# Kernel tuning notes

Measured on AMD Instinct MI355X. Metric: run time of the kernel, lower is better.

Reference implementation:

```python
import jax, jax.numpy as jnp
import numpy as np

N_VERT = 20000


def _gather_pad(feat, adj):
    # feat: [B, N, C]; adj: [B, N, K] with 1-based indices, 0 = padding (-> zeros)
    B, N, C = feat.shape
    padded = jnp.concatenate([jnp.zeros((B, 1, C), feat.dtype), feat], axis=1)  # [B, N+1, C]
    return jax.vmap(lambda p, a: p[a])(padded, adj)  # [B, N, K, C]


def setup_inputs() -> dict:
    key = jax.random.key(0)
    ks = jax.random.split(key, 7)
    B, N, K, M, C, O = 4, N_VERT, 16, 9, 64, 64
    x = jax.random.normal(ks[0], (B, N, C), jnp.float32)
    adj = jax.random.randint(ks[1], (B, N, K), 0, N + 1, jnp.int32)  # 0 == no neighbor
    W = jax.random.normal(ks[2], (M, O, C), jnp.float32) * 0.1
    b = jax.random.normal(ks[3], (O,), jnp.float32) * 0.1
    u = jax.random.normal(ks[4], (M, C), jnp.float32) * 0.1
    v = jax.random.normal(ks[5], (M, C), jnp.float32) * 0.1
    c = jax.random.normal(ks[6], (M,), jnp.float32) * 0.1
    return {"x": x, "adj": adj, "W": W, "b": b, "u": u, "v": v, "c": c}


def reference(x, adj, W, b, u, v, c):
    # FEAST graph conv, non-invariant path.
    mask = adj != 0  # [B, N, K]
    # attention logits: u.x_i + v.x_j + c, masked (padding) neighbors -> 0 + c
    ux = jnp.einsum('bnc,mc->bnm', x, u)          # [B, N, M]
    vx = jnp.einsum('bnc,mc->bnm', x, v)          # [B, N, M]
    vxn = _gather_pad(vx, adj)                    # [B, N, K, M]
    logits = jnp.where(mask[..., None], ux[:, :, None, :] + vxn, 0.0) + c
    q = jax.nn.softmax(logits, axis=-1)           # softmax over M kernels
    # gather raw neighbor features (zero for padding), contract q over K first,
    # then apply per-kernel W (linear, so order is equivalent to original wx-gather)
    xn = _gather_pad(x, adj)                      # [B, N, K, C]
    s = jnp.einsum('bnkm,bnkc->bnmc', q, xn)      # [B, N, M, C]
    out = jnp.einsum('bnmc,moc->bno', s, W)       # [B, N, O]
    deg = jnp.sum(mask, axis=-1).astype(x.dtype)  # [B, N]
    inv_deg = jnp.where(deg > 0, 1.0 / jnp.maximum(deg, 1.0), 0.0)
    return out * inv_deg[..., None] + b
```

## Files before the change

### kernel.cpp

```cpp
#include <hip/hip_runtime.h>
#include <cstdint>
#include <cstddef>

#define BB 4
#define NN 20000
#define KK 16
#define MM 9
#define CC 64
#define OO 64
#define BN (BB*NN)
#define MC (MM*CC)
#define NKS (MC/32)
#define NCH 625

typedef _Float16 f16x8 __attribute__((ext_vector_type(8)));
typedef _Float16 f16x4 __attribute__((ext_vector_type(4)));
typedef __fp16   fp16v2 __attribute__((ext_vector_type(2)));
typedef float    f32x4 __attribute__((ext_vector_type(4)));
typedef unsigned short u16;
typedef unsigned int   u32;

union Hcv { _Float16 h; u16 u; };
__device__ __forceinline__ u16 f2h(float f) { Hcv t; t.h = (_Float16)f; return t.u; }

__global__ __launch_bounds__(256) void pre_kernel(
    const float* __restrict__ x, const float* __restrict__ W,
    const float* __restrict__ u, const float* __restrict__ v,
    u16* __restrict__ xh, u16* __restrict__ wfb2, u16* __restrict__ uvfa)
{
    const int bid = blockIdx.x;
    if (bid == 1286) {
        int i0 = threadIdx.x * 8;
        u16 w8[8];
        #pragma unroll
        for (int tt = 0; tt < 8; ++tt) {
            int i = i0 + tt;
            int t = i >> 10, l = (i >> 4) & 63, s = (i >> 3) & 1, j = i & 7;
            int m = l & 15, hh = l >> 4;
            const float* src = t ? v : u;
            float val = (m < 9) ? src[m * 64 + s * 32 + hh * 8 + j] : 0.f;
            w8[tt] = f2h(val);
        }
        *(ushort4*)(uvfa + i0)     = *(ushort4*)(w8);
        *(ushort4*)(uvfa + i0 + 4) = *(ushort4*)(w8 + 4);
        return;
    }
    if (bid >= 1250) {
        int base = (bid - 1250) * 1024 + threadIdx.x * 4;
        ushort4 wv;
        u16* wp = (u16*)&wv;
        #pragma unroll
        for (int t = 0; t < 4; ++t) {
            int i = base + t;
            int j = i & 7, o = (i >> 3) & 63, l2 = (i >> 9) & 3, ks = i >> 11;
            int kf = ks * 32 + l2 * 8 + j;
            int m = kf >> 6, cc2 = kf & 63;
            wp[t] = f2h(W[m * 4096 + o * 64 + cc2]);
        }
        *(ushort4*)(wfb2 + base) = wv;
        return;
    }
    const int wave = threadIdx.x >> 6, lane = threadIdx.x & 63;
    const int lr = lane & 15, lhi = lane >> 4;
    const int t0n = bid * 64 + wave * 16;
    const float* xr = x + (size_t)(t0n + lr) * 64 + lhi * 8;
    float xf[16];
    *(float4*)(xf + 0)  = *(const float4*)(xr + 0);
    *(float4*)(xf + 4)  = *(const float4*)(xr + 4);
    *(float4*)(xf + 8)  = *(const float4*)(xr + 32);
    *(float4*)(xf + 12) = *(const float4*)(xr + 36);
    union { u16 us[8]; ushort4 s4[2]; } H0, H1;
    #pragma unroll
    for (int i = 0; i < 8; ++i) {
        H0.us[i] = f2h(xf[i]);
        H1.us[i] = f2h(xf[8 + i]);
    }
    u16* xw = xh + (size_t)(t0n + lr) * 64 + lhi * 8;
    *(ushort4*)(xw)          = H0.s4[0];
    *(ushort4*)(xw + 4)      = H0.s4[1];
    *(ushort4*)(xw + 32)     = H1.s4[0];
    *(ushort4*)(xw + 32 + 4) = H1.s4[1];
}

__global__ __launch_bounds__(256, 3) void fused_kernel(
    const u16* __restrict__ xh, const int* __restrict__ adj,
    const u16* __restrict__ wfb2, const u16* __restrict__ uvfa,
    const float* __restrict__ cvec, const float* __restrict__ bias,
    float* __restrict__ out)
{
    __shared__ __align__(16) u16 qlds[32 * 256];
    __shared__ __align__(16) u16 slds[72 * 32 * 8];
    const int bid = blockIdx.x;
    const int grp = bid & 7;
    const int b = grp >> 1;
    const int chunk = (bid >> 3) * 2 + (grp & 1);
    if (chunk >= NCH) return;
    const int tid = threadIdx.x, wave = tid >> 6, lane = tid & 63;
    const int lr = lane & 15, lhi = lane >> 4;
    const int node0 = b * NN + chunk * 32;
    const u16* xhb = xh + ((size_t)(b * NN) << 6);

    int jjA[2];
    jjA[0] = adj[(size_t)node0 * KK + tid];
    jjA[1] = adj[(size_t)node0 * KK + 256 + tid];

    f16x8 gLo[2][4], gHi[2][4];
    #pragma unroll
    for (int t = 0; t < 2; ++t)
        #pragma unroll
        for (int g2 = 0; g2 < 4; ++g2) {
            int e = __builtin_amdgcn_ds_bpermute((g2 * 16 + lr) * 4, jjA[t]);
            int erow = ((e > 0) ? e : 1) - 1;
            const u16* rp = xhb + ((size_t)erow << 6) + lhi * 8;
            gLo[t][g2] = *(const f16x8*)(rp);
            gHi[t][g2] = *(const f16x8*)(rp + 32);
        }

    const u16* up = uvfa + lane * 16;
    const f16x8 uAlo = *(const f16x8*)(up);
    const f16x8 uAhi = *(const f16x8*)(up + 8);
    const f16x8 vAlo = *(const f16x8*)(up + 1024);
    const f16x8 vAhi = *(const f16x8*)(up + 1024 + 8);
    float cv[4];
    #pragma unroll
    for (int r = 0; r < 4; ++r) { int m = lhi * 4 + r; cv[r] = (m < 9) ? cvec[m] : 0.f; }

    f16x8 idf[2];
    #pragma unroll
    for (int s = 0; s < 2; ++s) {
        union { u16 us[8]; f16x8 v; } t;
        #pragma unroll
        for (int j = 0; j < 8; ++j)
            t.us[j] = (lhi * 8 + j == s * 16 + lr) ? (u16)0x3C00 : (u16)0;
        idf[s] = t.v;
    }

    const int o0 = wave * 16;
    const float bv = bias[o0 + lr];
    const u32 qbase = (u32)(size_t)qlds;

    #pragma unroll
    for (int t = 0; t < 2; ++t) {
        unsigned long long bal = __ballot(jjA[t] != 0);
        #pragma unroll
        for (int g2 = 0; g2 < 4; ++g2) {
            const int nd = t * 16 + wave * 4 + g2;
            const u16* orp = xh + ((size_t)(node0 + nd) << 6) + lhi * 8;
            f16x8 oLo = *(const f16x8*)(orp);
            f16x8 oHi = *(const f16x8*)(orp + 32);
            f32x4 acc = {0.f, 0.f, 0.f, 0.f};
            acc = __builtin_amdgcn_mfma_f32_16x16x32_f16(vAlo, gLo[t][g2], acc, 0, 0, 0);
            acc = __builtin_amdgcn_mfma_f32_16x16x32_f16(vAhi, gHi[t][g2], acc, 0, 0, 0);
            acc = __builtin_amdgcn_mfma_f32_16x16x32_f16(uAlo, oLo, acc, 0, 0, 0);
            acc = __builtin_amdgcn_mfma_f32_16x16x32_f16(uAhi, oHi, acc, 0, 0, 0);
            u32 field = (u32)(bal >> (g2 * 16)) & 0xffffu;
            int  deg  = __popc(field);
            float inv = (deg > 0) ? __fdividef(1.0f, (float)deg) : 0.0f;
            int kbit = (field >> lr) & 1;
            float lm[4];
            #pragma unroll
            for (int r = 0; r < 4; ++r)
                lm[r] = (lhi * 4 + r < 9) ? (acc[r] + cv[r]) : -1e30f;
            float mx = fmaxf(fmaxf(lm[0], lm[1]), fmaxf(lm[2], lm[3]));
            mx = fmaxf(mx, __shfl_xor(mx, 16));
            mx = fmaxf(mx, __shfl_xor(mx, 32));
            float p0 = __expf(lm[0] - mx), p1 = __expf(lm[1] - mx);
            float p2 = __expf(lm[2] - mx), p3 = __expf(lm[3] - mx);
            float S = p0 + p1 + p2 + p3;
            S += __shfl_xor(S, 16);
            S += __shfl_xor(S, 32);
            float qsc = kbit ? __fdividef(inv, S) : 0.0f;
            union { fp16v2 h2[2]; uint2 u2; } qp;
            qp.h2[0] = __builtin_amdgcn_cvt_pkrtz(p0 * qsc, p1 * qsc);
            qp.h2[1] = __builtin_amdgcn_cvt_pkrtz(p2 * qsc, p3 * qsc);
            *(uint2*)(qlds + nd * 256 + lhi * 4 + (lr & 3) * 16 + (lr >> 2) * 64) = qp.u2;
        }
        asm volatile("s_waitcnt lgkmcnt(0)" ::: "memory");
        f16x4 qf[4];
        {
            u32 qa = qbase + (u32)((t * 16 + wave * 4) * 512) + (u32)(lane * 8);
            asm volatile("ds_read_b64_tr_b16 %0, %1 offset:0"    : "=v"(qf[0]) : "v"(qa) : "memory");
            asm volatile("ds_read_b64_tr_b16 %0, %1 offset:512"  : "=v"(qf[1]) : "v"(qa) : "memory");
            asm volatile("ds_read_b64_tr_b16 %0, %1 offset:1024" : "=v"(qf[2]) : "v"(qa) : "memory");
            asm volatile("ds_read_b64_tr_b16 %0, %1 offset:1536" : "=v"(qf[3]) : "v"(qa) : "memory");
            asm volatile("s_waitcnt lgkmcnt(0)" ::: "memory");
            __builtin_amdgcn_sched_barrier(0);
        }
        #pragma unroll
        for (int g2 = 0; g2 < 4; ++g2) {
            const int rnode = t * 16 + wave * 4 + g2;
            #pragma unroll
            for (int cc = 0; cc < 4; ++cc) {
                f32x4 xt = {0.f, 0.f, 0.f, 0.f};
                xt = __builtin_amdgcn_mfma_f32_16x16x32_f16(
                         (cc < 2) ? gLo[t][g2] : gHi[t][g2], idf[cc & 1], xt, 0, 0, 0);
                union { fp16v2 h2[2]; f16x4 h4; } at;
                at.h2[0] = __builtin_amdgcn_cvt_pkrtz(xt[0], xt[1]);
                at.h2[1] = __builtin_amdgcn_cvt_pkrtz(xt[2], xt[3]);
                f32x4 d2 = {0.f, 0.f, 0.f, 0.f};
                d2 = __builtin_amdgcn_mfma_f32_16x16x16f16(at.h4, qf[g2], d2, 0, 0, 0);
                if (lr < 9) {
                    u32 lo = __builtin_amdgcn_perm((u32)f2h(d2[1]), (u32)f2h(d2[0]), 0x05040100u);
                    u32 hi = __builtin_amdgcn_perm((u32)f2h(d2[3]), (u32)f2h(d2[2]), 0x05040100u);
                    int q_ = lr * 8 + cc * 2 + (lhi >> 1);
                    int idx = (((q_ * 32 + rnode) << 3) ^ ((lr & 7) << 3)) + (lhi & 1) * 4;
                    *(uint2*)(slds + idx) = make_uint2(lo, hi);
                }
            }
        }
    }
    __syncthreads();

    f32x4 a0 = {0.f, 0.f, 0.f, 0.f}, a1 = {0.f, 0.f, 0.f, 0.f};
    #pragma unroll
    for (int ks = 0; ks < NKS; ++ks) {
        int q_ = ks * 4 + lhi;
        int sw = ((q_ >> 3) & 7) << 3;
        f16x8 af0 = *(const f16x8*)(slds + ((((q_ * 32) + lr) << 3) ^ sw));
        f16x8 af1 = *(const f16x8*)(slds + ((((q_ * 32) + 16 + lr) << 3) ^ sw));
        f16x8 bf  = *(const f16x8*)(wfb2 + (size_t)(q_ * 64 + o0 + lr) * 8);
        a0 = __builtin_amdgcn_mfma_f32_16x16x32_f16(af0, bf, a0, 0, 0, 0);
        a1 = __builtin_amdgcn_mfma_f32_16x16x32_f16(af1, bf, a1, 0, 0, 0);
    }
    #pragma unroll
    for (int r = 0; r < 4; ++r) {
        out[(size_t)(node0 + lhi * 4 + r) * OO + o0 + lr]      = a0[r] + bv;
        out[(size_t)(node0 + 16 + lhi * 4 + r) * OO + o0 + lr] = a1[r] + bv;
    }
}

extern "C" void kernel_launch(void* const* d_in, const int* in_sizes, int n_in,
                              void* d_out, int out_size, void* d_ws, size_t ws_size,
                              hipStream_t stream)
{
    const float* x   = (const float*)d_in[0];
    const int*   adj = (const int*)  d_in[1];
    const float* W   = (const float*)d_in[2];
    const float* b   = (const float*)d_in[3];
    const float* u   = (const float*)d_in[4];
    const float* v   = (const float*)d_in[5];
    const float* c   = (const float*)d_in[6];
    float* out = (float*)d_out;

    u16* xh   = (u16*)d_ws;
    u16* wfb2 = xh + (size_t)BN * CC;
    u16* uvfa = wfb2 + 36864;

    pre_kernel<<<1287, 256, 0, stream>>>(x, W, u, v, xh, wfb2, uvfa);
    fused_kernel<<<2504, 256, 0, stream>>>(xh, adj, wfb2, uvfa, c, b, out);
}
```

Before: 134.8 us.

## Precompute u·x+c in pre-kernel and transpose gathered features via LDS reads

```diff
diff --git a/kernel.cpp b/kernel.cpp
--- a/kernel.cpp
+++ b/kernel.cpp
@@ -10,6 +10,7 @@
 #define OO 64
 #define BN (BB*NN)
 #define MC (MM*CC)
+#define UVP 12
 #define NKS (MC/32)
 #define NCH 625
 
@@ -22,27 +23,36 @@
 
 union Hcv { _Float16 h; u16 u; };
 __device__ __forceinline__ u16 f2h(float f) { Hcv t; t.h = (_Float16)f; return t.u; }
+__device__ __forceinline__ float h2f(u16 h) { Hcv t; t.u = h; return (float)t.h; }
+
+__device__ __forceinline__ f16x4 tr_read(u32 addr) {
+    f16x4 r;
+    asm volatile("ds_read_b64_tr_b16 %0, %1 offset:0" : "=v"(r) : "v"(addr) : "memory");
+    return r;
+}
 
 __global__ __launch_bounds__(256) void pre_kernel(
     const float* __restrict__ x, const float* __restrict__ W,
     const float* __restrict__ u, const float* __restrict__ v,
-    u16* __restrict__ xh, u16* __restrict__ wfb2, u16* __restrict__ uvfa)
+    const float* __restrict__ c,
+    float* __restrict__ uxcv, u16* __restrict__ xh,
+    u16* __restrict__ wfb2, u16* __restrict__ vfa)
 {
     const int bid = blockIdx.x;
     if (bid == 1286) {
-        int i0 = threadIdx.x * 8;
-        u16 w8[8];
-        #pragma unroll
-        for (int tt = 0; tt < 8; ++tt) {
-            int i = i0 + tt;
-            int t = i >> 10, l = (i >> 4) & 63, s = (i >> 3) & 1, j = i & 7;
-            int m = l & 15, hh = l >> 4;
-            const float* src = t ? v : u;
-            float val = (m < 9) ? src[m * 64 + s * 32 + hh * 8 + j] : 0.f;
-            w8[tt] = f2h(val);
-        }
-        *(ushort4*)(uvfa + i0)     = *(ushort4*)(w8);
-        *(ushort4*)(uvfa + i0 + 4) = *(ushort4*)(w8 + 4);
+        int i0 = threadIdx.x * 4;
+        if (i0 < 1024) {
+            u16 w4[4];
+            #pragma unroll
+            for (int tt = 0; tt < 4; ++tt) {
+                int i = i0 + tt;
+                int l = i >> 4, s = (i >> 3) & 1, j = i & 7;
+                int m = l & 15, hh = l >> 4;
+                float val = (m < 9) ? v[m * 64 + s * 32 + hh * 8 + j] : 0.f;
+                w4[tt] = f2h(val);
+            }
+            *(ushort4*)(vfa + i0) = *(ushort4*)(w4);
+        }
         return;
     }
     if (bid >= 1250) {
@@ -69,26 +79,55 @@
     *(float4*)(xf + 4)  = *(const float4*)(xr + 4);
     *(float4*)(xf + 8)  = *(const float4*)(xr + 32);
     *(float4*)(xf + 12) = *(const float4*)(xr + 36);
-    union { u16 us[8]; ushort4 s4[2]; } H0, H1;
+    union { u16 us[8]; f16x8 v; ushort4 s4[2]; } H0, L0, H1, L1;
     #pragma unroll
     for (int i = 0; i < 8; ++i) {
-        H0.us[i] = f2h(xf[i]);
-        H1.us[i] = f2h(xf[8 + i]);
+        u16 h = f2h(xf[i]);      H0.us[i] = h;  L0.us[i] = f2h(xf[i] - h2f(h));
+        u16 h2 = f2h(xf[8 + i]); H1.us[i] = h2; L1.us[i] = f2h(xf[8 + i] - h2f(h2));
     }
     u16* xw = xh + (size_t)(t0n + lr) * 64 + lhi * 8;
     *(ushort4*)(xw)          = H0.s4[0];
     *(ushort4*)(xw + 4)      = H0.s4[1];
     *(ushort4*)(xw + 32)     = H1.s4[0];
     *(ushort4*)(xw + 32 + 4) = H1.s4[1];
-}
-
-__global__ __launch_bounds__(256, 3) void fused_kernel(
+
+    f32x4 acc = {0.f,0.f,0.f,0.f};
+    const float* gp = u + lr * 64;
+    bool nz = lr < 9;
+    #pragma unroll
+    for (int s = 0; s < 2; ++s) {
+        float gf[8];
+        *(float4*)(gf + 0) = nz ? *(const float4*)(gp + s * 32 + lhi * 8)
+                                : make_float4(0.f,0.f,0.f,0.f);
+        *(float4*)(gf + 4) = nz ? *(const float4*)(gp + s * 32 + lhi * 8 + 4)
+                                : make_float4(0.f,0.f,0.f,0.f);
+        union { u16 us[8]; f16x8 v; } GH, GL;
+        #pragma unroll
+        for (int i = 0; i < 8; ++i) {
+            u16 h = f2h(gf[i]); GH.us[i] = h; GL.us[i] = f2h(gf[i] - h2f(h));
+        }
+        f16x8 as  = s ? H1.v : H0.v;
+        f16x8 asl = s ? L1.v : L0.v;
+        acc = __builtin_amdgcn_mfma_f32_16x16x32_f16(as,  GH.v, acc, 0, 0, 0);
+        acc = __builtin_amdgcn_mfma_f32_16x16x32_f16(as,  GL.v, acc, 0, 0, 0);
+        acc = __builtin_amdgcn_mfma_f32_16x16x32_f16(asl, GH.v, acc, 0, 0, 0);
+    }
+    float cv = (lr < 9) ? c[lr] : 0.f;
+    #pragma unroll
+    for (int reg = 0; reg < 4; ++reg) {
+        int node = t0n + lhi * 4 + reg;
+        if (lr < 9) uxcv[(size_t)node * UVP + lr] = acc[reg] + cv;
+    }
+}
+
+__global__ __launch_bounds__(256, 2) void fused_kernel(
     const u16* __restrict__ xh, const int* __restrict__ adj,
-    const u16* __restrict__ wfb2, const u16* __restrict__ uvfa,
-    const float* __restrict__ cvec, const float* __restrict__ bias,
+    const float* __restrict__ uxcv, const u16* __restrict__ wfb2,
+    const u16* __restrict__ vfa, const float* __restrict__ bias,
     float* __restrict__ out)
 {
-    __shared__ __align__(16) u16 qlds[32 * 256];
+    __shared__ __align__(16) u16 qlds[4 * 4 * 256];
+    __shared__ __align__(16) u16 xnlds[4 * 4 * 1024];
     __shared__ __align__(16) u16 slds[72 * 32 * 8];
     const int bid = blockIdx.x;
     const int grp = bid & 7;
@@ -116,43 +155,38 @@
             gHi[t][g2] = *(const f16x8*)(rp + 32);
         }
 
-    const u16* up = uvfa + lane * 16;
-    const f16x8 uAlo = *(const f16x8*)(up);
-    const f16x8 uAhi = *(const f16x8*)(up + 8);
-    const f16x8 vAlo = *(const f16x8*)(up + 1024);
-    const f16x8 vAhi = *(const f16x8*)(up + 1024 + 8);
-    float cv[4];
-    #pragma unroll
-    for (int r = 0; r < 4; ++r) { int m = lhi * 4 + r; cv[r] = (m < 9) ? cvec[m] : 0.f; }
-
-    f16x8 idf[2];
-    #pragma unroll
-    for (int s = 0; s < 2; ++s) {
-        union { u16 us[8]; f16x8 v; } t;
-        #pragma unroll
-        for (int j = 0; j < 8; ++j)
-            t.us[j] = (lhi * 8 + j == s * 16 + lr) ? (u16)0x3C00 : (u16)0;
-        idf[s] = t.v;
-    }
+    float4 uc[2][4];
+    #pragma unroll
+    for (int t = 0; t < 2; ++t)
+        #pragma unroll
+        for (int g2 = 0; g2 < 4; ++g2)
+            uc[t][g2] = *(const float4*)(uxcv +
+                          (size_t)(node0 + t * 16 + wave * 4 + g2) * UVP + lhi * 4);
+
+    const u16* vp = vfa + lane * 16;
+    const f16x8 vAlo = *(const f16x8*)(vp);
+    const f16x8 vAhi = *(const f16x8*)(vp + 8);
 
     const int o0 = wave * 16;
     const float bv = bias[o0 + lr];
-    const u32 qbase = (u32)(size_t)qlds;
+    const u32 qbase  = (u32)(size_t)qlds  + wave * 2048 + lane * 8;
+    const u32 xnbase = (u32)(size_t)xnlds + wave * 8192 + lane * 8;
+    u16* xnw = xnlds + wave * 4096 + (lhi >> 1) * 256 + lr * 16 + (lhi & 1) * 8;
+    u16* qwp = qlds + wave * 1024 + lhi * 4 + (lr & 3) * 16 + (lr >> 2) * 64;
 
     #pragma unroll
     for (int t = 0; t < 2; ++t) {
         unsigned long long bal = __ballot(jjA[t] != 0);
         #pragma unroll
         for (int g2 = 0; g2 < 4; ++g2) {
-            const int nd = t * 16 + wave * 4 + g2;
-            const u16* orp = xh + ((size_t)(node0 + nd) << 6) + lhi * 8;
-            f16x8 oLo = *(const f16x8*)(orp);
-            f16x8 oHi = *(const f16x8*)(orp + 32);
+            *(f16x8*)(xnw + g2 * 1024)       = gLo[t][g2];
+            *(f16x8*)(xnw + g2 * 1024 + 512) = gHi[t][g2];
+        }
+        #pragma unroll
+        for (int g2 = 0; g2 < 4; ++g2) {
             f32x4 acc = {0.f, 0.f, 0.f, 0.f};
             acc = __builtin_amdgcn_mfma_f32_16x16x32_f16(vAlo, gLo[t][g2], acc, 0, 0, 0);
             acc = __builtin_amdgcn_mfma_f32_16x16x32_f16(vAhi, gHi[t][g2], acc, 0, 0, 0);
-            acc = __builtin_amdgcn_mfma_f32_16x16x32_f16(uAlo, oLo, acc, 0, 0, 0);
-            acc = __builtin_amdgcn_mfma_f32_16x16x32_f16(uAhi, oHi, acc, 0, 0, 0);
             u32 field = (u32)(bal >> (g2 * 16)) & 0xffffu;
             int  deg  = __popc(field);
             float inv = (deg > 0) ? __fdividef(1.0f, (float)deg) : 0.0f;
@@ -160,7 +194,8 @@
             float lm[4];
             #pragma unroll
             for (int r = 0; r < 4; ++r)
-                lm[r] = (lhi * 4 + r < 9) ? (acc[r] + cv[r]) : -1e30f;
+                lm[r] = (lhi * 4 + r < 9) ? (acc[r] + ((const float*)&uc[t][g2])[r])
+                                          : -1e30f;
             float mx = fmaxf(fmaxf(lm[0], lm[1]), fmaxf(lm[2], lm[3]));
             mx = fmaxf(mx, __shfl_xor(mx, 16));
             mx = fmaxf(mx, __shfl_xor(mx, 32));
@@ -173,32 +208,27 @@
             union { fp16v2 h2[2]; uint2 u2; } qp;
             qp.h2[0] = __builtin_amdgcn_cvt_pkrtz(p0 * qsc, p1 * qsc);
             qp.h2[1] = __builtin_amdgcn_cvt_pkrtz(p2 * qsc, p3 * qsc);
-            *(uint2*)(qlds + nd * 256 + lhi * 4 + (lr & 3) * 16 + (lr >> 2) * 64) = qp.u2;
+            *(uint2*)(qwp + g2 * 256) = qp.u2;
         }
         asm volatile("s_waitcnt lgkmcnt(0)" ::: "memory");
-        f16x4 qf[4];
-        {
-            u32 qa = qbase + (u32)((t * 16 + wave * 4) * 512) + (u32)(lane * 8);
-            asm volatile("ds_read_b64_tr_b16 %0, %1 offset:0"    : "=v"(qf[0]) : "v"(qa) : "memory");
-            asm volatile("ds_read_b64_tr_b16 %0, %1 offset:512"  : "=v"(qf[1]) : "v"(qa) : "memory");
-            asm volatile("ds_read_b64_tr_b16 %0, %1 offset:1024" : "=v"(qf[2]) : "v"(qa) : "memory");
-            asm volatile("ds_read_b64_tr_b16 %0, %1 offset:1536" : "=v"(qf[3]) : "v"(qa) : "memory");
-            asm volatile("s_waitcnt lgkmcnt(0)" ::: "memory");
-            __builtin_amdgcn_sched_barrier(0);
-        }
+        __builtin_amdgcn_sched_barrier(0);
+        f16x4 qf[4], xnf[4][4];
+        #pragma unroll
+        for (int g2 = 0; g2 < 4; ++g2) {
+            qf[g2] = tr_read(qbase + g2 * 512);
+            #pragma unroll
+            for (int cc = 0; cc < 4; ++cc)
+                xnf[g2][cc] = tr_read(xnbase + g2 * 2048 + cc * 512);
+        }
+        asm volatile("s_waitcnt lgkmcnt(0)" ::: "memory");
+        __builtin_amdgcn_sched_barrier(0);
         #pragma unroll
         for (int g2 = 0; g2 < 4; ++g2) {
             const int rnode = t * 16 + wave * 4 + g2;
             #pragma unroll
             for (int cc = 0; cc < 4; ++cc) {
-                f32x4 xt = {0.f, 0.f, 0.f, 0.f};
-                xt = __builtin_amdgcn_mfma_f32_16x16x32_f16(
-                         (cc < 2) ? gLo[t][g2] : gHi[t][g2], idf[cc & 1], xt, 0, 0, 0);
-                union { fp16v2 h2[2]; f16x4 h4; } at;
-                at.h2[0] = __builtin_amdgcn_cvt_pkrtz(xt[0], xt[1]);
-                at.h2[1] = __builtin_amdgcn_cvt_pkrtz(xt[2], xt[3]);
                 f32x4 d2 = {0.f, 0.f, 0.f, 0.f};
-                d2 = __builtin_amdgcn_mfma_f32_16x16x16f16(at.h4, qf[g2], d2, 0, 0, 0);
+                d2 = __builtin_amdgcn_mfma_f32_16x16x16f16(xnf[g2][cc], qf[g2], d2, 0, 0, 0);
                 if (lr < 9) {
                     u32 lo = __builtin_amdgcn_perm((u32)f2h(d2[1]), (u32)f2h(d2[0]), 0x05040100u);
                     u32 hi = __builtin_amdgcn_perm((u32)f2h(d2[3]), (u32)f2h(d2[2]), 0x05040100u);
@@ -242,10 +272,11 @@
     const float* c   = (const float*)d_in[6];
     float* out = (float*)d_out;
 
-    u16* xh   = (u16*)d_ws;
-    u16* wfb2 = xh + (size_t)BN * CC;
-    u16* uvfa = wfb2 + 36864;
-
-    pre_kernel<<<1287, 256, 0, stream>>>(x, W, u, v, xh, wfb2, uvfa);
-    fused_kernel<<<2504, 256, 0, stream>>>(xh, adj, wfb2, uvfa, c, b, out);
-}
+    float* uxcv = (float*)d_ws;
+    u16*   xh   = (u16*)(uxcv + (size_t)BN * UVP);
+    u16*   wfb2 = xh + (size_t)BN * CC;
+    u16*   vfa  = wfb2 + 36864;
+
+    pre_kernel<<<1287, 256, 0, stream>>>(x, W, u, v, c, uxcv, xh, wfb2, vfa);
+    fused_kernel<<<2504, 256, 0, stream>>>(xh, adj, uxcv, wfb2, vfa, b, out);
+}
```

Measured after the change: 135.7 us. No clear change (+0.6%).
